# Kernel tuning notes

Hardware: AMD Instinct MI355X
Metric: run time of the kernel (lower is better)

Reference implementation:

```python
import jax, jax.numpy as jnp
import numpy as np

B, N, F, K, FILT = 256, 256, 128, 4, 256  # batch mols, max_atom, Fin, Chebyshev order, nb_filter
EPS = float(np.spacing(np.float32(0)))    # matches np.spacing(0) in original degree normalization
D2_FLOOR = 1e-12                          # numerical floor for sqrt of pairwise sq-dist


def setup_inputs() -> dict:
    key = jax.random.key(0)
    ks = jax.random.split(key, 6)
    x = jax.random.normal(ks[0], (B, N, F), dtype=jnp.float32)
    lap_in = 0.1 * jax.random.normal(ks[1], (B, N, N), dtype=jnp.float32)  # input per-mol Laplacian
    n_atoms = jax.random.randint(ks[2], (B,), 64, N + 1, dtype=jnp.int32)  # ragged mol sizes
    r1 = float(np.sqrt(6.0 / (F + F)))
    M_L = jax.random.uniform(ks[3], (F, F), jnp.float32, -r1, r1)          # Mahalanobis metric
    r2 = float(np.sqrt(6.0 / (F * K + FILT)))
    weight = jax.random.uniform(ks[4], (F * K, FILT), jnp.float32, -r2, r2)
    bias = jnp.zeros((FILT,), jnp.float32)
    return {"x": x, "lap_in": lap_in, "n_atoms": n_atoms, "M_L": M_L, "weight": weight, "bias": bias}


def reference(x, lap_in, n_atoms, M_L, weight, bias):
    # mask[b,n] = 1 for real atoms, 0 for padding (replaces per-mol tf.slice + pad)
    mask = (jnp.arange(N)[None, :] < n_atoms[:, None]).astype(x.dtype)       # [B,N]
    x = x * mask[..., None]

    # ---- learned Laplacian: Mahalanobis RBF affinity + sym degree normalization ----
    xw = jnp.einsum('bnf,fg->bng', x, M_L)                                   # x @ M_L
    sq = jnp.sum(xw * xw, axis=-1)                                           # [B,N]
    d2 = sq[:, :, None] + sq[:, None, :] - 2.0 * jnp.einsum('bif,bjf->bij', xw, xw)
    eye = jnp.eye(N, dtype=x.dtype)
    off = mask[:, :, None] * mask[:, None, :] * (1.0 - eye)                  # valid off-diag pairs
    d2_safe = jnp.where(off > 0, jnp.maximum(d2, D2_FLOOR), 1.0)
    W = jnp.exp(-jnp.sqrt(d2_safe)) * off                                    # W[i,j]=exp(-dist), diag 0
    deg = jnp.sum(W, axis=1) + EPS                                           # W symmetric: axis0==axis1
    dinv = jnp.where(mask > 0, 1.0 / jnp.sqrt(deg), 0.0)                     # D^{-1/2} (0 on padding)
    # L = I - D^{-1/2} W D^{-1/2} (intended math of the original py_func)
    L_learn = eye[None] * mask[:, :, None] - dinv[:, :, None] * W * dinv[:, None, :]
    L = L_learn + lap_in * (mask[:, :, None] * mask[:, None, :])             # L + sliced input LL

    # ---- Chebyshev recurrence: x0=x, x1=Lx, xk = 2 L x_{k-1} - x_{k-2} ----
    x0 = x
    x1 = jnp.einsum('bij,bjf->bif', L, x0)
    xs = [x0, x1]
    for _ in range(2, K):
        x2 = 2.0 * jnp.einsum('bij,bjf->bif', L, x1) - x0
        xs.append(x2)
        x0, x1 = x1, x2
    # stack -> [B,N,F,K] then flatten (f,k) row-major, matching reshape([K,M,F])->transpose([1,2,0])->reshape([M,K*F])
    xc = jnp.stack(xs, axis=-1).reshape(B, N, F * K)

    out = jnp.einsum('bnd,do->bno', xc, weight) + bias                       # [B,N,FILT]
    out = jax.nn.relu(out * mask[..., None])                                 # pad-to-max_atom + relu
    return out, L_learn
```

## Files before the change

### kernel.cpp

```cpp
#include <hip/hip_runtime.h>
#include <math.h>

typedef __bf16 bf16;
typedef __bf16 bf16x8 __attribute__((ext_vector_type(8)));
typedef __bf16 bf16x4 __attribute__((ext_vector_type(4)));
typedef float f32x4 __attribute__((ext_vector_type(4)));

constexpr int cB = 256, cN = 256, cF = 128, cO = 256;
constexpr int BN = cB * cN;
constexpr float D2_FLOOR = 1e-12f;
constexpr float EPS_F = 1.401298464324817e-45f;

constexpr size_t OFF_X0  = 0;
constexpr size_t OFF_X0T = OFF_X0 + (size_t)BN * 128 * 2;
constexpr size_t OFF_LB  = OFF_X0T + (size_t)cB * cF * cN * 2;
constexpr size_t OFF_WB  = OFF_LB + (size_t)cB * cN * cN * 2;
constexpr size_t OFF_WT  = OFF_WB + (size_t)cB * cN * cN * 2;
constexpr size_t OFF_MT  = OFF_WT + 512 * 256 * 2;
constexpr size_t OFF_DEG = OFF_MT + 128 * 128 * 2;

__device__ __forceinline__ bf16x8 gfrag(const bf16* __restrict__ p, int ld,
                                        int lane, int k0) {
  return *(const bf16x8*)(p + (size_t)(lane & 15) * ld + k0 + 8 * (lane >> 4));
}

__device__ __forceinline__ f32x4 mfma(bf16x8 a, bf16x8 b, f32x4 c) {
  return __builtin_amdgcn_mfma_f32_16x16x32_bf16(a, b, c, 0, 0, 0);
}

__device__ __forceinline__ void gll16(const void* g, void* l) {
  __builtin_amdgcn_global_load_lds((const __attribute__((address_space(1))) void*)g,
                                   (__attribute__((address_space(3))) void*)l, 16, 0, 0);
}

__global__ __launch_bounds__(256) void k_prep(const float* __restrict__ x,
                                              const int* __restrict__ na_p,
                                              bf16* __restrict__ X0,
                                              bf16* __restrict__ x0T) {
  __shared__ __align__(16) bf16 T[64][132];
  int b = blockIdx.x >> 2, i0 = (blockIdx.x & 3) * 64;
  int tid = threadIdx.x;
  int na = na_p[b];
#pragma unroll
  for (int it = 0; it < 8; ++it) {
    int ir = it * 8 + (tid >> 5);
    int f0 = (tid & 31) * 4;
    int i = i0 + ir;
    float m = (i < na) ? 1.f : 0.f;
    float4 v = *(const float4*)(x + ((size_t)b * cN + i) * cF + f0);
    bf16x4 pk = {(bf16)(v.x * m), (bf16)(v.y * m), (bf16)(v.z * m), (bf16)(v.w * m)};
    *(bf16x4*)(X0 + ((size_t)b * cN + i) * cF + f0) = pk;
    *(bf16x4*)(&T[ir][f0]) = pk;
  }
  __syncthreads();
  int f = tid >> 1, half = tid & 1;
  bf16* od = x0T + ((size_t)b * cF + f) * cN + i0 + half * 32;
#pragma unroll
  for (int c = 0; c < 32; c += 4) {
    int ii = half * 32 + c;
    bf16x4 pk = {T[ii][f], T[ii + 1][f], T[ii + 2][f], T[ii + 3][f]};
    *(bf16x4*)(od + c) = pk;
  }
}

__global__ __launch_bounds__(256) void k_wt(const float* __restrict__ wgt,
                                            const float* __restrict__ ML,
                                            bf16* __restrict__ Wt,
                                            bf16* __restrict__ MT) {
  int id = blockIdx.x * 256 + threadIdx.x;
  if (id < 512 * 256) {
    int o = id >> 9, d = id & 511;
    int k = d >> 7, f = d & 127;
    Wt[id] = (bf16)wgt[(f * 4 + k) * 256 + o];
  } else {
    int id2 = id - 512 * 256;
    if (id2 < 128 * 128) {
      int g = id2 >> 7, f = id2 & 127;
      MT[id2] = (bf16)ML[f * 128 + g];
    }
  }
}

__global__ __launch_bounds__(512, 2) void k_xwgram(const bf16* __restrict__ X0,
                                                   const bf16* __restrict__ MT,
                                                   const int* __restrict__ na_p,
                                                   bf16* __restrict__ Wb16,
                                                   float* __restrict__ deg) {
  __shared__ __align__(16) char XW[65536];
  __shared__ float lsq[256];
  int bx = blockIdx.x;
  int b = bx >> 1, h = bx & 1;
  int tid = threadIdx.x, wid = tid >> 6, lane = tid & 63;
  int hi = lane >> 4, il = lane & 15;

  const bf16* A = X0 + ((size_t)b * cN + wid * 32) * cF;
  f32x4 acc[2][8] = {};
#pragma unroll
  for (int ks = 0; ks < 4; ++ks) {
    int k0 = ks * 32;
    bf16x8 a0 = gfrag(A, cF, lane, k0);
    bf16x8 a1 = gfrag(A + 16 * cF, cF, lane, k0);
#pragma unroll
    for (int gt = 0; gt < 8; ++gt) {
      bf16x8 bb = gfrag(MT + (size_t)gt * 16 * 128, 128, lane, k0);
      acc[0][gt] = mfma(a0, bb, acc[0][gt]);
      acc[1][gt] = mfma(a1, bb, acc[1][gt]);
    }
  }
#pragma unroll
  for (int nt = 0; nt < 2; ++nt) {
#pragma unroll
    for (int r = 0; r < 4; ++r) {
      int n = 32 * wid + 16 * nt + 4 * hi + r;
      int swz = (n & 7) << 4;
      float s = 0.f;
#pragma unroll
      for (int gt = 0; gt < 8; ++gt) {
        bf16 v = (bf16)acc[nt][gt][r];
        *(bf16*)(XW + n * 256 + ((2 * (16 * gt + il)) ^ swz)) = v;
        float f = (float)v;
        s = fmaf(f, f, s);
      }
      s += __shfl_xor(s, 1); s += __shfl_xor(s, 2);
      s += __shfl_xor(s, 4); s += __shfl_xor(s, 8);
      if (il == 0) lsq[n] = s;
    }
  }
  __syncthreads();

  int ibase = h * 128 + 16 * wid;
  int ia = ibase + il;
  f32x4 g2[16] = {};
#pragma unroll
  for (int ks = 0; ks < 4; ++ks) {
    int cb = 64 * ks + 16 * hi;
    bf16x8 af = *(const bf16x8*)(XW + ia * 256 + (cb ^ ((ia & 7) << 4)));
#pragma unroll
    for (int jt = 0; jt < 16; ++jt) {
      int j = 16 * jt + il;
      bf16x8 bf_ = *(const bf16x8*)(XW + j * 256 + (cb ^ ((j & 7) << 4)));
      g2[jt] = mfma(af, bf_, g2[jt]);
    }
  }
  int na = na_p[b];
#pragma unroll
  for (int r = 0; r < 4; ++r) {
    int i = ibase + 4 * hi + r;
    float sqi = lsq[i];
    bool mi = i < na;
    float rs = 0.f;
#pragma unroll
    for (int jt = 0; jt < 16; ++jt) {
      int j = 16 * jt + il;
      float w = 0.f;
      if (mi && j < na && i != j) {
        float d2 = fmaxf(sqi + lsq[j] - 2.f * g2[jt][r], D2_FLOOR);
        w = __expf(-sqrtf(d2));
      }
      Wb16[((size_t)b * cN + i) * cN + j] = (bf16)w;
      rs += w;
    }
    rs += __shfl_xor(rs, 1); rs += __shfl_xor(rs, 2);
    rs += __shfl_xor(rs, 4); rs += __shfl_xor(rs, 8);
    if (il == 0) deg[b * cN + i] = rs;
  }
}

__global__ __launch_bounds__(256) void k_Lassm(const bf16* __restrict__ Wb16,
                                               const float* __restrict__ deg,
                                               const float* __restrict__ lap,
                                               const int* __restrict__ na_p,
                                               bf16* __restrict__ Lb,
                                               float* __restrict__ llearn) {
  int tid = threadIdx.x;
  size_t e = ((size_t)blockIdx.x * 256 + tid) * 8;
  int b = (int)(e >> 16);
  int na = na_p[b];
  __shared__ float dinvl[256];
  dinvl[tid] = (tid < na) ? 1.f / sqrtf(deg[b * cN + tid] + EPS_F) : 0.f;
  __syncthreads();
  int j = (int)(e & 255);
  int i = (int)((e >> 8) & 255);
  bf16x8 w8 = *(const bf16x8*)(Wb16 + e);
  float4 lp0 = *(const float4*)(lap + e);
  float4 lp1 = *(const float4*)(lap + e + 4);
  float di = dinvl[i];
  float mi = (i < na) ? 1.f : 0.f;
  float4 ll0, ll1;
  bf16x8 lo;
#pragma unroll
  for (int c = 0; c < 8; ++c) {
    int jj = j + c;
    float v = -di * (float)w8[c] * dinvl[jj];
    if (i == jj && i < na) v += 1.f;
    float lpv = (c < 4) ? (&lp0.x)[c] : (&lp1.x)[c - 4];
    if (c < 4) (&ll0.x)[c] = v; else (&ll1.x)[c - 4] = v;
    float mj = (jj < na) ? 1.f : 0.f;
    lo[c] = (bf16)(v + lpv * mi * mj);
  }
  *(float4*)(llearn + e) = ll0;
  *(float4*)(llearn + e + 4) = ll1;
  *(bf16x8*)(Lb + e) = lo;
}

__device__ __forceinline__ void cheb_pass(const bf16* __restrict__ Lm,
                                          const char* Bsrc, const char* Ppp,
                                          char* Odst, int wid, int lane, bool haspp) {
  int hi = lane >> 4, il = lane & 15;
  int i0w = wid * 32;
  f32x4 acc[2][8] = {};
#pragma unroll
  for (int ks = 0; ks < 8; ++ks) {
    int k0 = ks * 32;
    bf16x8 a0 = gfrag(Lm + (size_t)i0w * cN, cN, lane, k0);
    bf16x8 a1 = gfrag(Lm + (size_t)(i0w + 16) * cN, cN, lane, k0);
#pragma unroll
    for (int nf = 0; nf < 8; ++nf) {
      int f = nf * 16 + il;
      const char* p = Bsrc + f * 512 + ((64 * ks + 16 * hi) ^ ((il & 7) << 4));
      bf16x8 bb = *(const bf16x8*)p;
      acc[0][nf] = mfma(a0, bb, acc[0][nf]);
      acc[1][nf] = mfma(a1, bb, acc[1][nf]);
    }
  }
#pragma unroll
  for (int mf = 0; mf < 2; ++mf) {
    int ib = i0w + mf * 16 + 4 * hi;
#pragma unroll
    for (int nf = 0; nf < 8; ++nf) {
      int f = nf * 16 + il;
      int cb = (2 * ib) ^ ((il & 7) << 4);
      bf16x4 o;
      if (haspp) {
        bf16x4 pp = *(const bf16x4*)(Ppp + f * 512 + cb);
#pragma unroll
        for (int r = 0; r < 4; ++r) o[r] = (bf16)(2.f * acc[mf][nf][r] - (float)pp[r]);
      } else {
#pragma unroll
        for (int r = 0; r < 4; ++r) o[r] = (bf16)acc[mf][nf][r];
      }
      *(bf16x4*)(Odst + f * 512 + cb) = o;
    }
  }
}

__global__ __launch_bounds__(512) void k_chebout(const bf16* __restrict__ x0T,
                                                 const bf16* __restrict__ Lb,
                                                 const bf16* __restrict__ Wt,
                                                 const float* __restrict__ bias,
                                                 const int* __restrict__ na_p,
                                                 float* __restrict__ out) {
  __shared__ __align__(16) char XB[2][65536];
  int b = blockIdx.x;
  int tid = threadIdx.x, wid = tid >> 6, lane = tid & 63;
  int hi = lane >> 4, il = lane & 15;
  const bf16* Lm = Lb + (size_t)b * cN * cN;
  const char* src = (const char*)(x0T + (size_t)b * cF * cN);

  f32x4 oacc[2][16] = {};

#pragma unroll
  for (int it = 0; it < 8; ++it) {
    int beta = it * 8192 + tid * 16;
    int f = beta >> 9, c = beta & 511;
    gll16(src + f * 512 + (c ^ ((f & 7) << 4)), XB[0] + beta);
  }
  __syncthreads();

#define SLICE(Bsrc, kst)                                                         \
  {                                                                              \
    const char* sb_ = (Bsrc);                                                    \
    _Pragma("unroll")                                                            \
    for (int ftp = 0; ftp < 4; ++ftp) {                                          \
      bf16x8 av[2];                                                              \
      _Pragma("unroll")                                                          \
      for (int nt = 0; nt < 2; ++nt) {                                           \
        int i_ = wid * 32 + nt * 16 + il;                                        \
        _Pragma("unroll")                                                        \
        for (int j = 0; j < 8; ++j) {                                            \
          int f_ = 32 * ftp + 8 * hi + j;                                        \
          av[nt][j] = *(const bf16*)(sb_ + f_ * 512 + ((2 * i_) ^ (j << 4)));    \
        }                                                                        \
      }                                                                          \
      _Pragma("unroll")                                                          \
      for (int ot = 0; ot < 16; ++ot) {                                          \
        bf16x8 bb = gfrag(Wt + (size_t)(16 * ot) * 512, 512, lane,               \
                          (kst) * 128 + 32 * ftp);                               \
        oacc[0][ot] = mfma(av[0], bb, oacc[0][ot]);                              \
        oacc[1][ot] = mfma(av[1], bb, oacc[1][ot]);                              \
      }                                                                          \
    }                                                                            \
  }

  SLICE(XB[0], 0);
  cheb_pass(Lm, XB[0], nullptr, XB[1], wid, lane, false);
  SLICE(XB[1], 1);
  __syncthreads();
  cheb_pass(Lm, XB[1], XB[0], XB[0], wid, lane, true);
  SLICE(XB[0], 2);
  __syncthreads();
  cheb_pass(Lm, XB[0], XB[1], XB[1], wid, lane, true);
  SLICE(XB[1], 3);
#undef SLICE

  int na = na_p[b];
#pragma unroll
  for (int ot = 0; ot < 16; ++ot) {
    int o = 16 * ot + il;
    float bo = bias[o];
#pragma unroll
    for (int nt = 0; nt < 2; ++nt) {
#pragma unroll
      for (int r = 0; r < 4; ++r) {
        int n = wid * 32 + nt * 16 + 4 * hi + r;
        float m = (n < na) ? 1.f : 0.f;
        out[((size_t)b * cN + n) * cO + o] = fmaxf((oacc[nt][ot][r] + bo) * m, 0.f);
      }
    }
  }
}

extern "C" void kernel_launch(void* const* d_in, const int* in_sizes, int n_in,
                              void* d_out, int out_size, void* d_ws, size_t ws_size,
                              hipStream_t stream) {
  const float* x    = (const float*)d_in[0];
  const float* lap  = (const float*)d_in[1];
  const int*   na   = (const int*)d_in[2];
  const float* M_L  = (const float*)d_in[3];
  const float* wgt  = (const float*)d_in[4];
  const float* bias = (const float*)d_in[5];

  float* out    = (float*)d_out;
  float* llearn = out + (size_t)BN * cO;

  char* ws = (char*)d_ws;
  bf16*  X0  = (bf16*)(ws + OFF_X0);
  bf16*  x0T = (bf16*)(ws + OFF_X0T);
  bf16*  Lb  = (bf16*)(ws + OFF_LB);
  bf16*  Wb  = (bf16*)(ws + OFF_WB);
  bf16*  Wt  = (bf16*)(ws + OFF_WT);
  bf16*  MT  = (bf16*)(ws + OFF_MT);
  float* deg = (float*)(ws + OFF_DEG);

  k_prep<<<dim3(1024), 256, 0, stream>>>(x, na, X0, x0T);
  k_wt<<<dim3(576), 256, 0, stream>>>(wgt, M_L, Wt, MT);
  k_xwgram<<<dim3(512), 512, 0, stream>>>(X0, MT, na, Wb, deg);
  k_Lassm<<<dim3(8192), 256, 0, stream>>>(Wb, deg, lap, na, Lb, llearn);
  k_chebout<<<dim3(cB), 512, 0, stream>>>(x0T, Lb, Wt, bias, na, out);
}
```

Measured before the change: 408.1 us.

## Fuse prep, Gram, Laplacian assembly and Chebyshev into one per-molecule kernel

Replaces four kernels (masking/transpose, xW Gram with W write, L assembly, Chebyshev+output) with a single kernel, one 512-thread block per molecule. x is masked and transposed in LDS, and xW is built in LDS. The Gram matrix is computed twice, once for degrees and once for L, so the bf16 W matrix, the degree vector and the X0/x0T buffers never go through global memory. In exchange it does redundant MFMA/exp work. Grid parallelism drops to 256 blocks, and the llearn, lap and Lb accesses become narrow scalar per-lane stores and loads, which may underuse bandwidth.

```diff
diff --git a/kernel.cpp b/kernel.cpp
--- a/kernel.cpp
+++ b/kernel.cpp
@@ -11,56 +11,23 @@
 constexpr float D2_FLOOR = 1e-12f;
 constexpr float EPS_F = 1.401298464324817e-45f;
 
-constexpr size_t OFF_X0  = 0;
-constexpr size_t OFF_X0T = OFF_X0 + (size_t)BN * 128 * 2;
-constexpr size_t OFF_LB  = OFF_X0T + (size_t)cB * cF * cN * 2;
-constexpr size_t OFF_WB  = OFF_LB + (size_t)cB * cN * cN * 2;
-constexpr size_t OFF_WT  = OFF_WB + (size_t)cB * cN * cN * 2;
-constexpr size_t OFF_MT  = OFF_WT + 512 * 256 * 2;
-constexpr size_t OFF_DEG = OFF_MT + 128 * 128 * 2;
+constexpr size_t OFF_LB = 0;
+constexpr size_t OFF_WT = OFF_LB + (size_t)cB * cN * cN * 2;
+constexpr size_t OFF_MT = OFF_WT + 512 * 256 * 2;
 
 __device__ __forceinline__ bf16x8 gfrag(const bf16* __restrict__ p, int ld,
                                         int lane, int k0) {
   return *(const bf16x8*)(p + (size_t)(lane & 15) * ld + k0 + 8 * (lane >> 4));
 }
 
+__device__ __forceinline__ bf16x8 lfragB(const char* base, int row0, int k0, int lane) {
+  int row = row0 + (lane & 15);
+  return *(const bf16x8*)(base + row * 256 +
+                          ((2 * (k0 + 8 * (lane >> 4))) ^ ((row & 7) << 4)));
+}
+
 __device__ __forceinline__ f32x4 mfma(bf16x8 a, bf16x8 b, f32x4 c) {
   return __builtin_amdgcn_mfma_f32_16x16x32_bf16(a, b, c, 0, 0, 0);
-}
-
-__device__ __forceinline__ void gll16(const void* g, void* l) {
-  __builtin_amdgcn_global_load_lds((const __attribute__((address_space(1))) void*)g,
-                                   (__attribute__((address_space(3))) void*)l, 16, 0, 0);
-}
-
-__global__ __launch_bounds__(256) void k_prep(const float* __restrict__ x,
-                                              const int* __restrict__ na_p,
-                                              bf16* __restrict__ X0,
-                                              bf16* __restrict__ x0T) {
-  __shared__ __align__(16) bf16 T[64][132];
-  int b = blockIdx.x >> 2, i0 = (blockIdx.x & 3) * 64;
-  int tid = threadIdx.x;
-  int na = na_p[b];
-#pragma unroll
-  for (int it = 0; it < 8; ++it) {
-    int ir = it * 8 + (tid >> 5);
-    int f0 = (tid & 31) * 4;
-    int i = i0 + ir;
-    float m = (i < na) ? 1.f : 0.f;
-    float4 v = *(const float4*)(x + ((size_t)b * cN + i) * cF + f0);
-    bf16x4 pk = {(bf16)(v.x * m), (bf16)(v.y * m), (bf16)(v.z * m), (bf16)(v.w * m)};
-    *(bf16x4*)(X0 + ((size_t)b * cN + i) * cF + f0) = pk;
-    *(bf16x4*)(&T[ir][f0]) = pk;
-  }
-  __syncthreads();
-  int f = tid >> 1, half = tid & 1;
-  bf16* od = x0T + ((size_t)b * cF + f) * cN + i0 + half * 32;
-#pragma unroll
-  for (int c = 0; c < 32; c += 4) {
-    int ii = half * 32 + c;
-    bf16x4 pk = {T[ii][f], T[ii + 1][f], T[ii + 2][f], T[ii + 3][f]};
-    *(bf16x4*)(od + c) = pk;
-  }
 }
 
 __global__ __launch_bounds__(256) void k_wt(const float* __restrict__ wgt,
@@ -81,128 +48,6 @@
   }
 }
 
-__global__ __launch_bounds__(512, 2) void k_xwgram(const bf16* __restrict__ X0,
-                                                   const bf16* __restrict__ MT,
-                                                   const int* __restrict__ na_p,
-                                                   bf16* __restrict__ Wb16,
-                                                   float* __restrict__ deg) {
-  __shared__ __align__(16) char XW[65536];
-  __shared__ float lsq[256];
-  int bx = blockIdx.x;
-  int b = bx >> 1, h = bx & 1;
-  int tid = threadIdx.x, wid = tid >> 6, lane = tid & 63;
-  int hi = lane >> 4, il = lane & 15;
-
-  const bf16* A = X0 + ((size_t)b * cN + wid * 32) * cF;
-  f32x4 acc[2][8] = {};
-#pragma unroll
-  for (int ks = 0; ks < 4; ++ks) {
-    int k0 = ks * 32;
-    bf16x8 a0 = gfrag(A, cF, lane, k0);
-    bf16x8 a1 = gfrag(A + 16 * cF, cF, lane, k0);
-#pragma unroll
-    for (int gt = 0; gt < 8; ++gt) {
-      bf16x8 bb = gfrag(MT + (size_t)gt * 16 * 128, 128, lane, k0);
-      acc[0][gt] = mfma(a0, bb, acc[0][gt]);
-      acc[1][gt] = mfma(a1, bb, acc[1][gt]);
-    }
-  }
-#pragma unroll
-  for (int nt = 0; nt < 2; ++nt) {
-#pragma unroll
-    for (int r = 0; r < 4; ++r) {
-      int n = 32 * wid + 16 * nt + 4 * hi + r;
-      int swz = (n & 7) << 4;
-      float s = 0.f;
-#pragma unroll
-      for (int gt = 0; gt < 8; ++gt) {
-        bf16 v = (bf16)acc[nt][gt][r];
-        *(bf16*)(XW + n * 256 + ((2 * (16 * gt + il)) ^ swz)) = v;
-        float f = (float)v;
-        s = fmaf(f, f, s);
-      }
-      s += __shfl_xor(s, 1); s += __shfl_xor(s, 2);
-      s += __shfl_xor(s, 4); s += __shfl_xor(s, 8);
-      if (il == 0) lsq[n] = s;
-    }
-  }
-  __syncthreads();
-
-  int ibase = h * 128 + 16 * wid;
-  int ia = ibase + il;
-  f32x4 g2[16] = {};
-#pragma unroll
-  for (int ks = 0; ks < 4; ++ks) {
-    int cb = 64 * ks + 16 * hi;
-    bf16x8 af = *(const bf16x8*)(XW + ia * 256 + (cb ^ ((ia & 7) << 4)));
-#pragma unroll
-    for (int jt = 0; jt < 16; ++jt) {
-      int j = 16 * jt + il;
-      bf16x8 bf_ = *(const bf16x8*)(XW + j * 256 + (cb ^ ((j & 7) << 4)));
-      g2[jt] = mfma(af, bf_, g2[jt]);
-    }
-  }
-  int na = na_p[b];
-#pragma unroll
-  for (int r = 0; r < 4; ++r) {
-    int i = ibase + 4 * hi + r;
-    float sqi = lsq[i];
-    bool mi = i < na;
-    float rs = 0.f;
-#pragma unroll
-    for (int jt = 0; jt < 16; ++jt) {
-      int j = 16 * jt + il;
-      float w = 0.f;
-      if (mi && j < na && i != j) {
-        float d2 = fmaxf(sqi + lsq[j] - 2.f * g2[jt][r], D2_FLOOR);
-        w = __expf(-sqrtf(d2));
-      }
-      Wb16[((size_t)b * cN + i) * cN + j] = (bf16)w;
-      rs += w;
-    }
-    rs += __shfl_xor(rs, 1); rs += __shfl_xor(rs, 2);
-    rs += __shfl_xor(rs, 4); rs += __shfl_xor(rs, 8);
-    if (il == 0) deg[b * cN + i] = rs;
-  }
-}
-
-__global__ __launch_bounds__(256) void k_Lassm(const bf16* __restrict__ Wb16,
-                                               const float* __restrict__ deg,
-                                               const float* __restrict__ lap,
-                                               const int* __restrict__ na_p,
-                                               bf16* __restrict__ Lb,
-                                               float* __restrict__ llearn) {
-  int tid = threadIdx.x;
-  size_t e = ((size_t)blockIdx.x * 256 + tid) * 8;
-  int b = (int)(e >> 16);
-  int na = na_p[b];
-  __shared__ float dinvl[256];
-  dinvl[tid] = (tid < na) ? 1.f / sqrtf(deg[b * cN + tid] + EPS_F) : 0.f;
-  __syncthreads();
-  int j = (int)(e & 255);
-  int i = (int)((e >> 8) & 255);
-  bf16x8 w8 = *(const bf16x8*)(Wb16 + e);
-  float4 lp0 = *(const float4*)(lap + e);
-  float4 lp1 = *(const float4*)(lap + e + 4);
-  float di = dinvl[i];
-  float mi = (i < na) ? 1.f : 0.f;
-  float4 ll0, ll1;
-  bf16x8 lo;
-#pragma unroll
-  for (int c = 0; c < 8; ++c) {
-    int jj = j + c;
-    float v = -di * (float)w8[c] * dinvl[jj];
-    if (i == jj && i < na) v += 1.f;
-    float lpv = (c < 4) ? (&lp0.x)[c] : (&lp1.x)[c - 4];
-    if (c < 4) (&ll0.x)[c] = v; else (&ll1.x)[c - 4] = v;
-    float mj = (jj < na) ? 1.f : 0.f;
-    lo[c] = (bf16)(v + lpv * mi * mj);
-  }
-  *(float4*)(llearn + e) = ll0;
-  *(float4*)(llearn + e + 4) = ll1;
-  *(bf16x8*)(Lb + e) = lo;
-}
-
 __device__ __forceinline__ void cheb_pass(const bf16* __restrict__ Lm,
                                           const char* Bsrc, const char* Ppp,
                                           char* Odst, int wid, int lane, bool haspp) {
@@ -244,28 +89,155 @@
   }
 }
 
-__global__ __launch_bounds__(512) void k_chebout(const bf16* __restrict__ x0T,
-                                                 const bf16* __restrict__ Lb,
+__global__ __launch_bounds__(512, 1) void k_mega(const float* __restrict__ x,
+                                                 const float* __restrict__ lap,
+                                                 const int* __restrict__ na_p,
+                                                 const bf16* __restrict__ MT,
                                                  const bf16* __restrict__ Wt,
                                                  const float* __restrict__ bias,
-                                                 const int* __restrict__ na_p,
-                                                 float* __restrict__ out) {
-  __shared__ __align__(16) char XB[2][65536];
+                                                 bf16* __restrict__ Lb,
+                                                 float* __restrict__ out,
+                                                 float* __restrict__ llearn) {
+  __shared__ __align__(16) char bufA[65536];
+  __shared__ __align__(16) char bufB[65536];
+  __shared__ float lsq[256];
+  __shared__ float dinvl[256];
   int b = blockIdx.x;
   int tid = threadIdx.x, wid = tid >> 6, lane = tid & 63;
   int hi = lane >> 4, il = lane & 15;
-  const bf16* Lm = Lb + (size_t)b * cN * cN;
-  const char* src = (const char*)(x0T + (size_t)b * cF * cN);
+  int na = na_p[b];
+  const float* xb = x + (size_t)b * cN * cF;
+
+#pragma unroll
+  for (int it = 0; it < 16; ++it) {
+    int e = (tid + it * 512) * 4;
+    int n = e >> 7, f0 = e & 127;
+    float m = (n < na) ? 1.f : 0.f;
+    float4 v = *(const float4*)(xb + e);
+    bf16x4 pk = {(bf16)(v.x * m), (bf16)(v.y * m), (bf16)(v.z * m), (bf16)(v.w * m)};
+    *(bf16x4*)(bufB + n * 256 + ((2 * f0) ^ ((n & 7) << 4))) = pk;
+  }
+  __syncthreads();
+
+#pragma unroll
+  for (int it = 0; it < 16; ++it) {
+    int u = tid + it * 512;
+    int f = u & 127, i0 = 4 * (u >> 7);
+    bf16x4 pk;
+#pragma unroll
+    for (int r = 0; r < 4; ++r) {
+      int n = i0 + r;
+      pk[r] = *(const bf16*)(bufB + n * 256 + ((2 * f) ^ ((n & 7) << 4)));
+    }
+    *(bf16x4*)(bufA + f * 512 + ((2 * i0) ^ ((f & 7) << 4))) = pk;
+  }
+  __syncthreads();
+
+  {
+    f32x4 acc[2][8] = {};
+#pragma unroll
+    for (int ks = 0; ks < 4; ++ks) {
+      int k0 = ks * 32;
+      bf16x8 a0 = lfragB(bufB, 32 * wid, k0, lane);
+      bf16x8 a1 = lfragB(bufB, 32 * wid + 16, k0, lane);
+#pragma unroll
+      for (int gt = 0; gt < 8; ++gt) {
+        bf16x8 bb = gfrag(MT + (size_t)gt * 16 * 128, 128, lane, k0);
+        acc[0][gt] = mfma(a0, bb, acc[0][gt]);
+        acc[1][gt] = mfma(a1, bb, acc[1][gt]);
+      }
+    }
+#pragma unroll
+    for (int nt = 0; nt < 2; ++nt) {
+#pragma unroll
+      for (int r = 0; r < 4; ++r) {
+        int n = 32 * wid + 16 * nt + 4 * hi + r;
+        int swz = (n & 7) << 4;
+        float s = 0.f;
+#pragma unroll
+        for (int gt = 0; gt < 8; ++gt) {
+          bf16 v = (bf16)acc[nt][gt][r];
+          *(bf16*)(bufB + n * 256 + ((2 * (16 * gt + il)) ^ swz)) = v;
+          float f = (float)v;
+          s = fmaf(f, f, s);
+        }
+        s += __shfl_xor(s, 1); s += __shfl_xor(s, 2);
+        s += __shfl_xor(s, 4); s += __shfl_xor(s, 8);
+        if (il == 0) lsq[n] = s;
+      }
+    }
+  }
+  __syncthreads();
+
+#pragma unroll
+  for (int ih = 0; ih < 2; ++ih) {
+    int n0 = 32 * wid + 16 * ih;
+    f32x4 g2[16] = {};
+#pragma unroll
+    for (int ks = 0; ks < 4; ++ks) {
+      int k0 = ks * 32;
+      bf16x8 af = lfragB(bufB, n0, k0, lane);
+#pragma unroll
+      for (int jt = 0; jt < 16; ++jt)
+        g2[jt] = mfma(af, lfragB(bufB, 16 * jt, k0, lane), g2[jt]);
+    }
+#pragma unroll
+    for (int r = 0; r < 4; ++r) {
+      int i = n0 + 4 * hi + r;
+      float sqi = lsq[i];
+      bool mi = i < na;
+      float rs = 0.f;
+#pragma unroll
+      for (int jt = 0; jt < 16; ++jt) {
+        int j = 16 * jt + il;
+        if (mi && j < na && i != j)
+          rs += __expf(-sqrtf(fmaxf(sqi + lsq[j] - 2.f * g2[jt][r], D2_FLOOR)));
+      }
+      rs += __shfl_xor(rs, 1); rs += __shfl_xor(rs, 2);
+      rs += __shfl_xor(rs, 4); rs += __shfl_xor(rs, 8);
+      if (il == 0) dinvl[i] = mi ? 1.f / sqrtf(rs + EPS_F) : 0.f;
+    }
+  }
+  __syncthreads();
+
+  const float* lapb = lap + (size_t)b * cN * cN;
+  float* llb = llearn + (size_t)b * cN * cN;
+  bf16* lbb = Lb + (size_t)b * cN * cN;
+#pragma unroll
+  for (int ih = 0; ih < 2; ++ih) {
+    int n0 = 32 * wid + 16 * ih;
+    f32x4 g2[16] = {};
+#pragma unroll
+    for (int ks = 0; ks < 4; ++ks) {
+      int k0 = ks * 32;
+      bf16x8 af = lfragB(bufB, n0, k0, lane);
+#pragma unroll
+      for (int jt = 0; jt < 16; ++jt)
+        g2[jt] = mfma(af, lfragB(bufB, 16 * jt, k0, lane), g2[jt]);
+    }
+#pragma unroll
+    for (int r = 0; r < 4; ++r) {
+      int i = n0 + 4 * hi + r;
+      float sqi = lsq[i];
+      bool mi = i < na;
+      float di = dinvl[i];
+      float mif = mi ? 1.f : 0.f;
+#pragma unroll
+      for (int jt = 0; jt < 16; ++jt) {
+        int j = 16 * jt + il;
+        float w = 0.f;
+        if (mi && j < na && i != j)
+          w = __expf(-sqrtf(fmaxf(sqi + lsq[j] - 2.f * g2[jt][r], D2_FLOOR)));
+        float v = -di * w * dinvl[j];
+        if (i == j && mi) v += 1.f;
+        llb[(size_t)i * cN + j] = v;
+        float mjf = (j < na) ? 1.f : 0.f;
+        lbb[(size_t)i * cN + j] = (bf16)(v + lapb[(size_t)i * cN + j] * mif * mjf);
+      }
+    }
+  }
 
   f32x4 oacc[2][16] = {};
-
-#pragma unroll
-  for (int it = 0; it < 8; ++it) {
-    int beta = it * 8192 + tid * 16;
-    int f = beta >> 9, c = beta & 511;
-    gll16(src + f * 512 + (c ^ ((f & 7) << 4)), XB[0] + beta);
-  }
-  __syncthreads();
 
 #define SLICE(Bsrc, kst)                                                         \
   {                                                                              \
@@ -292,18 +264,19 @@
     }                                                                            \
   }
 
-  SLICE(XB[0], 0);
-  cheb_pass(Lm, XB[0], nullptr, XB[1], wid, lane, false);
-  SLICE(XB[1], 1);
-  __syncthreads();
-  cheb_pass(Lm, XB[1], XB[0], XB[0], wid, lane, true);
-  SLICE(XB[0], 2);
-  __syncthreads();
-  cheb_pass(Lm, XB[0], XB[1], XB[1], wid, lane, true);
-  SLICE(XB[1], 3);
+  SLICE(bufA, 0);
+  __syncthreads();
+
+  cheb_pass(lbb, bufA, nullptr, bufB, wid, lane, false);
+  SLICE(bufB, 1);
+  __syncthreads();
+  cheb_pass(lbb, bufB, bufA, bufA, wid, lane, true);
+  SLICE(bufA, 2);
+  __syncthreads();
+  cheb_pass(lbb, bufA, bufB, bufB, wid, lane, true);
+  SLICE(bufB, 3);
 #undef SLICE
 
-  int na = na_p[b];
 #pragma unroll
   for (int ot = 0; ot < 16; ++ot) {
     int o = 16 * ot + il;
@@ -334,17 +307,10 @@
   float* llearn = out + (size_t)BN * cO;
 
   char* ws = (char*)d_ws;
-  bf16*  X0  = (bf16*)(ws + OFF_X0);
-  bf16*  x0T = (bf16*)(ws + OFF_X0T);
-  bf16*  Lb  = (bf16*)(ws + OFF_LB);
-  bf16*  Wb  = (bf16*)(ws + OFF_WB);
-  bf16*  Wt  = (bf16*)(ws + OFF_WT);
-  bf16*  MT  = (bf16*)(ws + OFF_MT);
-  float* deg = (float*)(ws + OFF_DEG);
-
-  k_prep<<<dim3(1024), 256, 0, stream>>>(x, na, X0, x0T);
+  bf16* Lb = (bf16*)(ws + OFF_LB);
+  bf16* Wt = (bf16*)(ws + OFF_WT);
+  bf16* MT = (bf16*)(ws + OFF_MT);
+
   k_wt<<<dim3(576), 256, 0, stream>>>(wgt, M_L, Wt, MT);
-  k_xwgram<<<dim3(512), 512, 0, stream>>>(X0, MT, na, Wb, deg);
-  k_Lassm<<<dim3(8192), 256, 0, stream>>>(Wb, deg, lap, na, Lb, llearn);
-  k_chebout<<<dim3(cB), 512, 0, stream>>>(x0T, Lb, Wt, bias, na, out);
-}
+  k_mega<<<dim3(cB), 512, 0, stream>>>(x, lap, na, MT, Wt, bias, Lb, out, llearn);
+}
```

Result: slower. 431.6 us (+5.8%).
